# Performance work log

Hardware: AMD Instinct MI355X
Metric: run time of the kernel (lower is better)

## Reference

```python
import jax, jax.numpy as jnp
import numpy as np

D_MODEL = 2048
N_HEADS = 16
D_K = D_MODEL // N_HEADS
D_FF = 5504
SEQ = 4096
CONTEXT_LENGTH = 4096
THETA = 10000.0
EPS = 1e-5


def _linear(x, w):
    # w: (out, in), matches torch einsum '...i,oi->...o'
    return jnp.einsum('...i,oi->...o', x, w)


def _rmsnorm(x, g):
    xf = x.astype(jnp.float32)
    rms = jnp.sqrt(jnp.mean(xf * xf, axis=-1, keepdims=True) + EPS)
    return (xf / rms * g).astype(x.dtype)


def _rope_tables():
    powers = jnp.arange(0, D_K, 2, dtype=jnp.float32) / D_K
    freqs = 1.0 / (THETA ** powers)                       # (D_K/2,)
    t = jnp.arange(CONTEXT_LENGTH, dtype=jnp.float32)
    ang = jnp.outer(t, freqs)                             # (ctx, D_K/2)
    return jnp.cos(ang), jnp.sin(ang)


def _apply_rope(x, token_positions, cos_c, sin_c):
    # x: (b, h, s, d_k); token_positions: (b, s)
    cos = cos_c[token_positions][None].astype(x.dtype)    # (1, b, s, d_k/2)
    sin = sin_c[token_positions][None].astype(x.dtype)
    x_even = x[..., ::2]
    x_odd = x[..., 1::2]
    r1 = x_even * cos - x_odd * sin
    r2 = x_even * sin + x_odd * cos
    # interleave back: (..., d_k/2, 2) -> (..., d_k)
    out = jnp.stack([r1, r2], axis=-1)
    return out.reshape(x.shape)


def setup_inputs() -> dict:
    key = jax.random.key(0)
    ks = jax.random.split(key, 12)

    def w(k, out_f, in_f):
        std = (2.0 / (in_f + out_f)) ** 0.5
        return std * jax.random.normal(k, (out_f, in_f), dtype=jnp.float32)

    return {
        'x': jax.random.normal(ks[0], (1, SEQ, D_MODEL), dtype=jnp.float32),
        'w_q': w(ks[1], D_MODEL, D_MODEL),
        'w_k': w(ks[2], D_MODEL, D_MODEL),
        'w_v': w(ks[3], D_MODEL, D_MODEL),
        'w_o': w(ks[4], D_MODEL, D_MODEL),
        'w1': w(ks[5], D_FF, D_MODEL),
        'w2': w(ks[6], D_MODEL, D_FF),
        'w3': w(ks[7], D_FF, D_MODEL),
        'g1': jnp.ones((D_MODEL,), dtype=jnp.float32),
        'g2': jnp.ones((D_MODEL,), dtype=jnp.float32),
        'token_positions': jnp.broadcast_to(jnp.arange(SEQ, dtype=jnp.int32)[None, :], (1, SEQ)),
    }


def reference(x, w_q, w_k, w_v, w_o, w1, w2, w3, g1, g2, token_positions):
    b, s, _ = x.shape
    cos_c, sin_c = _rope_tables()

    # --- pre-norm attention ---
    xn = _rmsnorm(x, g1)
    def heads(t):
        return t.reshape(b, s, N_HEADS, D_K).transpose(0, 2, 1, 3)  # (b,h,s,d)
    q = heads(_linear(xn, w_q))
    k = heads(_linear(xn, w_k))
    v = heads(_linear(xn, w_v))
    q = _apply_rope(q, token_positions, cos_c, sin_c)
    k = _apply_rope(k, token_positions, cos_c, sin_c)

    score = jnp.einsum('bhqd,bhkd->bhqk', q, k) / (D_K ** 0.5)
    causal = jnp.tril(jnp.ones((s, s), dtype=bool))
    score = jnp.where(causal, score, -jnp.inf)
    probs = jax.nn.softmax(score, axis=-1)
    attn = jnp.einsum('bhqk,bhkd->bhqd', probs, v)
    attn = attn.transpose(0, 2, 1, 3).reshape(b, s, D_MODEL)
    x = x + _linear(attn, w_o)

    # --- pre-norm SwiGLU FFN ---
    xn = _rmsnorm(x, g2)
    gate = _linear(xn, w1)
    gate = gate * jax.nn.sigmoid(gate)  # SiLU
    x = x + _linear(gate * _linear(xn, w3), w2)
    return x
```

## Files before the change

kernel.cpp:

```cpp
#include <hip/hip_runtime.h>
#include <hip/hip_bf16.h>
#include <cstdint>
#include <cstddef>

constexpr int S_   = 4096;
constexpr int DM   = 2048;
constexpr int NH   = 16;
constexpr int DK   = 128;
constexpr int DFF  = 5504;
constexpr int DFFP = 5632;
constexpr int QLD  = 3 * DM;

typedef float  f32x4 __attribute__((ext_vector_type(4)));
typedef short  s16x8 __attribute__((ext_vector_type(8)));
typedef __bf16 bfx8  __attribute__((ext_vector_type(8)));

template <typename T, typename U>
__device__ inline auto mfma_try(T a, T b, f32x4 c, int)
    -> decltype(__builtin_amdgcn_mfma_f32_16x16x32_bf16(a, b, c, 0, 0, 0)) {
  return __builtin_amdgcn_mfma_f32_16x16x32_bf16(a, b, c, 0, 0, 0);
}
template <typename T, typename U>
__device__ inline f32x4 mfma_try(T a, T b, f32x4 c, long) {
  U a2 = __builtin_bit_cast(U, a);
  U b2 = __builtin_bit_cast(U, b);
  return __builtin_amdgcn_mfma_f32_16x16x32_bf16(a2, b2, c, 0, 0, 0);
}
__device__ __forceinline__ f32x4 MFMA_BF16(s16x8 a, s16x8 b, f32x4 c) {
  return mfma_try<s16x8, bfx8>(a, b, c, 0);
}

__device__ __forceinline__ void async_ld16(void* lds, const void* g) {
  __builtin_amdgcn_global_load_lds(
      (__attribute__((address_space(1))) void*)(g),
      (__attribute__((address_space(3))) void*)(lds), 16, 0, 0);
}

__device__ __forceinline__ float bf2f(__hip_bfloat16 h) { return __bfloat162float(h); }
__device__ __forceinline__ __hip_bfloat16 f2bf(float f) { return __float2bfloat16(f); }

__global__ __launch_bounds__(256) void cvt_kernel(const float* __restrict__ in,
                                                  __hip_bfloat16* __restrict__ out, int n) {
  int i = (blockIdx.x * 256 + threadIdx.x) * 4;
  if (i >= n) return;
  float4 v = *reinterpret_cast<const float4*>(in + i);
  union { __hip_bfloat16 h[4]; uint2 u; } pk;
  pk.h[0] = f2bf(v.x); pk.h[1] = f2bf(v.y); pk.h[2] = f2bf(v.z); pk.h[3] = f2bf(v.w);
  *reinterpret_cast<uint2*>(out + i) = pk.u;
}

__global__ __launch_bounds__(256) void cvt_pad_kernel(const float* __restrict__ in,
                                                      __hip_bfloat16* __restrict__ out,
                                                      int n_src, int n_tot) {
  int i = (blockIdx.x * 256 + threadIdx.x) * 4;
  if (i >= n_tot) return;
  union { __hip_bfloat16 h[4]; uint2 u; } pk;
  if (i < n_src) {
    float4 v = *reinterpret_cast<const float4*>(in + i);
    pk.h[0] = f2bf(v.x); pk.h[1] = f2bf(v.y); pk.h[2] = f2bf(v.z); pk.h[3] = f2bf(v.w);
  } else {
    pk.u.x = 0u; pk.u.y = 0u;
  }
  *reinterpret_cast<uint2*>(out + i) = pk.u;
}

__global__ __launch_bounds__(256) void rmsnorm_kernel(const float* __restrict__ x,
                                                      const float* __restrict__ g,
                                                      __hip_bfloat16* __restrict__ out) {
  const int row = blockIdx.x, tid = threadIdx.x;
  const float4* xr = reinterpret_cast<const float4*>(x + (size_t)row * DM);
  float4 a = xr[tid], b = xr[tid + 256];
  float ss = a.x*a.x + a.y*a.y + a.z*a.z + a.w*a.w
           + b.x*b.x + b.y*b.y + b.z*b.z + b.w*b.w;
#pragma unroll
  for (int off = 1; off < 64; off <<= 1) ss += __shfl_xor(ss, off);
  __shared__ float red[4];
  if ((tid & 63) == 0) red[tid >> 6] = ss;
  __syncthreads();
  const float inv = rsqrtf((red[0] + red[1] + red[2] + red[3]) * (1.0f / DM) + 1e-5f);
  const float4* gr = reinterpret_cast<const float4*>(g);
  float4 ga = gr[tid], gb = gr[tid + 256];
  union { __hip_bfloat16 h[4]; uint2 u; } pa, pb;
  pa.h[0] = f2bf(a.x * inv * ga.x); pa.h[1] = f2bf(a.y * inv * ga.y);
  pa.h[2] = f2bf(a.z * inv * ga.z); pa.h[3] = f2bf(a.w * inv * ga.w);
  pb.h[0] = f2bf(b.x * inv * gb.x); pb.h[1] = f2bf(b.y * inv * gb.y);
  pb.h[2] = f2bf(b.z * inv * gb.z); pb.h[3] = f2bf(b.w * inv * gb.w);
  uint2* o = reinterpret_cast<uint2*>(out + (size_t)row * DM);
  o[tid] = pa.u; o[tid + 256] = pb.u;
}

__global__ __launch_bounds__(256) void rope_kernel(__hip_bfloat16* __restrict__ t,
                                                   const int* __restrict__ pos, int col0) {
  const size_t idx = (size_t)blockIdx.x * 256 + threadIdx.x;
  const int j = (int)(idx & 63);
  const int h = (int)((idx >> 6) & 15);
  const int s = (int)(idx >> 10);
  const float p = (float)pos[s];
  const float freq = exp2f((float)j * (-13.287712379549449f / 64.0f));
  float sn, cs;
  sincosf(p * freq, &sn, &cs);
  __hip_bfloat16* ptr = t + (size_t)s * QLD + col0 + h * DK + 2 * j;
  const float e = bf2f(ptr[0]), o = bf2f(ptr[1]);
  ptr[0] = f2bf(e * cs - o * sn);
  ptr[1] = f2bf(e * sn + o * cs);
}

__global__ __launch_bounds__(256) void transpose_v(const __hip_bfloat16* __restrict__ qkv,
                                                   __hip_bfloat16* __restrict__ vt) {
  __shared__ __hip_bfloat16 tile[64][65];
  const int h = blockIdx.z;
  const int s0 = blockIdx.x * 64, d0 = blockIdx.y * 64;
  const int lane = threadIdx.x & 63, w = threadIdx.x >> 6;
#pragma unroll
  for (int i = 0; i < 16; i++) {
    const int r = w * 16 + i;
    tile[r][lane] = qkv[(size_t)(s0 + r) * QLD + 2 * DM + h * DK + d0 + lane];
  }
  __syncthreads();
#pragma unroll
  for (int i = 0; i < 16; i++) {
    const int r = w * 16 + i;
    vt[(size_t)(h * DK + d0 + r) * S_ + s0 + lane] = tile[lane][r];
  }
}

enum { EP_BF16 = 0, EP_SILU = 1, EP_MUL = 2, EP_ADDF32 = 3 };

template <int EP>
__global__ __launch_bounds__(512, 2) void gemm2(const __hip_bfloat16* __restrict__ A,
                                                const __hip_bfloat16* __restrict__ B,
                                                int N, int K, int lda, int ldb,
                                                void* outp, const void* extra) {
  __shared__ char lds[3][24576];
  const int tid = threadIdx.x;
  const int wave = tid >> 6, lane = tid & 63;
  const int l15 = lane & 15, l4 = lane >> 4;
  const int wm = wave >> 2, wn = wave & 3;

  const int nbn = gridDim.x;
  const int nwg = gridDim.x * gridDim.y;
  int lin = blockIdx.y * gridDim.x + blockIdx.x;
  if ((nwg & 7) == 0) lin = (lin & 7) * (nwg >> 3) + (lin >> 3);
  const int bm = (lin / nbn) * 128;
  const int bn = (lin % nbn) * 256;

  const int NT = K >> 5;

  const int srcCh = ((tid & 3) ^ ((tid >> 3) & 3)) * 16;
  const char* Asrc  = (const char*)A + (size_t)(bm + (tid >> 2)) * lda * 2 + srcCh;
  const char* Bsrc0 = (const char*)B + (size_t)(bn + (tid >> 2)) * ldb * 2 + srcCh;
  const char* Bsrc1 = (const char*)B + (size_t)(bn + 128 + (tid >> 2)) * ldb * 2 + srcCh;
  char* const ldsA  = &lds[0][0] + wave * 1024;
  char* const ldsB0 = &lds[0][0] + 8192 + wave * 1024;
  char* const ldsB1 = &lds[0][0] + 16384 + wave * 1024;

  auto stage_a  = [&](int t, int s) { async_ld16(ldsA  + s * 24576, Asrc  + (size_t)t * 64); };
  auto stage_b0 = [&](int t, int s) { async_ld16(ldsB0 + s * 24576, Bsrc0 + (size_t)t * 64); };
  auto stage_b1 = [&](int t, int s) { async_ld16(ldsB1 + s * 24576, Bsrc1 + (size_t)t * 64); };

  const int rdch = (l4 ^ ((l15 >> 1) & 3)) * 16;
  auto rd_a = [&](int s, int mq, int f) -> s16x8 {
    return *(const s16x8*)(&lds[s][0] + (wm * 64 + mq * 32 + f * 16 + l15) * 64 + rdch);
  };
  auto rd_b = [&](int s, int nf) -> s16x8 {
    return *(const s16x8*)(&lds[s][8192] + (wn * 64 + nf * 16 + l15) * 64 + rdch);
  };

  f32x4 acc[4][4] = {};

  stage_a(0, 0); stage_b0(0, 0); stage_b1(0, 0);
  stage_a(1, 1); stage_b0(1, 1); stage_b1(1, 1);

  for (int t = 0; t < NT; t++) {
    const int s = t % 3;
    if (t + 1 < NT) { asm volatile("s_waitcnt vmcnt(3)" ::: "memory"); }
    else            { asm volatile("s_waitcnt vmcnt(0)" ::: "memory"); }
    __builtin_amdgcn_s_barrier();
    asm volatile("" ::: "memory");
    s16x8 b0 = rd_b(s, 0), b1 = rd_b(s, 1), b2 = rd_b(s, 2), b3 = rd_b(s, 3);
    s16x8 a0 = rd_a(s, 0, 0), a1 = rd_a(s, 0, 1);
    if (t + 2 < NT) { const int s2 = (t + 2) % 3; stage_a(t + 2, s2); stage_b0(t + 2, s2); }
    __builtin_amdgcn_s_barrier();
    asm volatile("" ::: "memory");
    __builtin_amdgcn_s_setprio(1);
    acc[0][0] = MFMA_BF16(a0, b0, acc[0][0]);
    acc[0][1] = MFMA_BF16(a0, b1, acc[0][1]);
    acc[0][2] = MFMA_BF16(a0, b2, acc[0][2]);
    acc[0][3] = MFMA_BF16(a0, b3, acc[0][3]);
    acc[1][0] = MFMA_BF16(a1, b0, acc[1][0]);
    acc[1][1] = MFMA_BF16(a1, b1, acc[1][1]);
    acc[1][2] = MFMA_BF16(a1, b2, acc[1][2]);
    acc[1][3] = MFMA_BF16(a1, b3, acc[1][3]);
    __builtin_amdgcn_s_setprio(0);
    s16x8 a2 = rd_a(s, 1, 0), a3 = rd_a(s, 1, 1);
    if (t + 2 < NT) stage_b1(t + 2, (t + 2) % 3);
    __builtin_amdgcn_s_barrier();
    asm volatile("" ::: "memory");
    __builtin_amdgcn_s_setprio(1);
    acc[2][0] = MFMA_BF16(a2, b0, acc[2][0]);
    acc[2][1] = MFMA_BF16(a2, b1, acc[2][1]);
    acc[2][2] = MFMA_BF16(a2, b2, acc[2][2]);
    acc[2][3] = MFMA_BF16(a2, b3, acc[2][3]);
    acc[3][0] = MFMA_BF16(a3, b0, acc[3][0]);
    acc[3][1] = MFMA_BF16(a3, b1, acc[3][1]);
    acc[3][2] = MFMA_BF16(a3, b2, acc[3][2]);
    acc[3][3] = MFMA_BF16(a3, b3, acc[3][3]);
    __builtin_amdgcn_s_setprio(0);
  }

#pragma unroll
  for (int mf = 0; mf < 4; mf++)
#pragma unroll
    for (int nf = 0; nf < 4; nf++)
#pragma unroll
      for (int r = 0; r < 4; r++) {
        const int row = bm + wm * 64 + mf * 16 + l4 * 4 + r;
        const int col = bn + wn * 64 + nf * 16 + l15;
        const size_t idx = (size_t)row * N + col;
        const float v = acc[mf][nf][r];
        if constexpr (EP == EP_BF16) {
          ((__hip_bfloat16*)outp)[idx] = f2bf(v);
        } else if constexpr (EP == EP_SILU) {
          ((__hip_bfloat16*)outp)[idx] = f2bf(v / (1.0f + __expf(-v)));
        } else if constexpr (EP == EP_MUL) {
          const float o = bf2f(((const __hip_bfloat16*)extra)[idx]);
          ((__hip_bfloat16*)outp)[idx] = f2bf(v * o);
        } else {
          ((float*)outp)[idx] = v + ((const float*)extra)[idx];
        }
      }
}

__global__ __launch_bounds__(512, 4) void attn_kernel(const __hip_bfloat16* __restrict__ qkv,
                                                      const __hip_bfloat16* __restrict__ vt,
                                                      __hip_bfloat16* __restrict__ out) {
  __shared__ char sKb[2][64 * 256];
  __shared__ char sVb[2][128 * 128];
  __shared__ char sPb[8][16 * 64];

  const int h = blockIdx.y;
  const int qtile = gridDim.x - 1 - blockIdx.x;
  const int q0 = qtile * 128;
  const int tid = threadIdx.x, wave = tid >> 6, lane = tid & 63;
  const int l15 = lane & 15, l4 = lane >> 4;
  const int qr0 = q0 + wave * 16;
  const int ntiles = qtile * 2 + 2;

  s16x8 qf[4];
  {
    const char* src = (const char*)qkv + (((size_t)(qr0 + l15)) * QLD + h * DK + l4 * 8) * 2;
#pragma unroll
    for (int ks = 0; ks < 4; ks++) qf[ks] = *(const s16x8*)(src + ks * 64);
  }

  const char* qkvK = (const char*)qkv + ((size_t)DM + h * DK) * 2;
  const char* vtH  = (const char*)vt;

  auto stage = [&](int t, int buf) {
    const int kv0 = t * 64;
#pragma unroll
    for (int a = 0; a < 2; a++) {
      const int rl = wave * 8 + a * 4 + l4;
      const int ck = l15 ^ ((a * 4 + l4) & 7);
      async_ld16(sKb[buf] + (wave * 8 + a * 4) * 256,
                 qkvK + (size_t)(kv0 + rl) * (QLD * 2) + ck * 16);
    }
#pragma unroll
    for (int a = 0; a < 2; a++) {
      const int rl = wave * 16 + a * 8 + (lane >> 3);
      const int cv = (lane & 7) ^ (lane >> 3);
      async_ld16(sVb[buf] + (wave * 16 + a * 8) * 128,
                 vtH + ((size_t)(h * DK + rl) * S_ + kv0) * 2 + cv * 16);
    }
  };

  f32x4 acc[8] = {};
  float m_ = -__builtin_inff(), l_ = 0.f;
  const float scale = 0.08838834764831845f;

  stage(0, 0);
  asm volatile("s_waitcnt vmcnt(0)" ::: "memory");
  __syncthreads();

  unsigned* sPw32 = (unsigned*)sPb[wave];
  const char* sPw = (const char*)sPb[wave];

  for (int t = 0; t < ntiles; t++) {
    const int cur = t & 1;
    if (t + 1 < ntiles) stage(t + 1, cur ^ 1);
    const char* Kt = sKb[cur];
    const char* Vt = sVb[cur];
    const int kv0 = t * 64;

#pragma unroll
    for (int hf = 0; hf < 2; hf++) {
      f32x4 st[2] = {};
#pragma unroll
      for (int sub = 0; sub < 2; sub++)
#pragma unroll
        for (int ks = 0; ks < 4; ks++) {
          s16x8 kf = *(const s16x8*)(Kt + (hf * 32 + sub * 16 + l15) * 256 +
                                     (((ks * 4 + l4) ^ (l15 & 7)) & 15) * 16);
          st[sub] = MFMA_BF16(kf, qf[ks], st[sub]);
        }
      const int qrow = qr0 + l15;
      const int kvb = kv0 + hf * 32;
      float p[8];
      float mx = -__builtin_inff();
#pragma unroll
      for (int sub = 0; sub < 2; sub++)
#pragma unroll
        for (int r = 0; r < 4; r++) {
          const int kv = kvb + sub * 16 + l4 * 4 + r;
          const float v = st[sub][r] * scale;
          const float pv = (kv <= qrow) ? v : -__builtin_inff();
          p[sub * 4 + r] = pv;
          mx = fmaxf(mx, pv);
        }
      mx = fmaxf(mx, __shfl_xor(mx, 16));
      mx = fmaxf(mx, __shfl_xor(mx, 32));
      const float nm = fmaxf(m_, mx);
      const float alpha = __expf(m_ - nm);
      m_ = nm;
      float psum = 0.f;
#pragma unroll
      for (int i = 0; i < 8; i++) {
        p[i] = __expf(p[i] - nm);
        psum += p[i];
      }
      psum += __shfl_xor(psum, 16);
      psum += __shfl_xor(psum, 32);
      l_ = l_ * alpha + psum;

#pragma unroll
      for (int sub = 0; sub < 2; sub++)
#pragma unroll
        for (int rp = 0; rp < 2; rp++) {
          union { __hip_bfloat16 hh[2]; unsigned u; } pk;
          pk.hh[0] = f2bf(p[sub * 4 + rp * 2]);
          pk.hh[1] = f2bf(p[sub * 4 + rp * 2 + 1]);
          sPw32[l15 * 16 + sub * 8 + l4 * 2 + rp] = pk.u;
        }
#pragma unroll
      for (int nt = 0; nt < 8; nt++)
#pragma unroll
        for (int r = 0; r < 4; r++) acc[nt][r] *= alpha;

      s16x8 pa = *(const s16x8*)(sPw + l15 * 64 + l4 * 16);
#pragma unroll
      for (int nt = 0; nt < 8; nt++) {
        s16x8 vb = *(const s16x8*)(Vt + (nt * 16 + l15) * 128 +
                                   (((hf * 4 + l4) ^ (l15 & 7)) & 7) * 16);
        acc[nt] = MFMA_BF16(vb, pa, acc[nt]);
      }
    }
    asm volatile("s_waitcnt vmcnt(0)" ::: "memory");
    __syncthreads();
  }

  const float rl = 1.0f / l_;
#pragma unroll
  for (int nt = 0; nt < 8; nt++) {
    union { __hip_bfloat16 hh[4]; uint2 u; } pk;
#pragma unroll
    for (int r = 0; r < 4; r++) pk.hh[r] = f2bf(acc[nt][r] * rl);
    *reinterpret_cast<uint2*>(out + (size_t)(qr0 + l15) * DM + h * DK + nt * 16 + l4 * 4) = pk.u;
  }
}

extern "C" void kernel_launch(void* const* d_in, const int* in_sizes, int n_in,
                              void* d_out, int out_size, void* d_ws, size_t ws_size,
                              hipStream_t stream) {
  const float* x   = (const float*)d_in[0];
  const float* w_q = (const float*)d_in[1];
  const float* w_k = (const float*)d_in[2];
  const float* w_v = (const float*)d_in[3];
  const float* w_o = (const float*)d_in[4];
  const float* w1  = (const float*)d_in[5];
  const float* w2  = (const float*)d_in[6];
  const float* w3  = (const float*)d_in[7];
  const float* g1  = (const float*)d_in[8];
  const float* g2  = (const float*)d_in[9];
  const int*   tp  = (const int*)d_in[10];
  float* outf = (float*)d_out;

  constexpr size_t SZ_WQKV  = (size_t)3 * DM * DM * 2;
  constexpr size_t OFF_ATTN = (size_t)DM * DM * 2;
  constexpr size_t OFF_XN   = SZ_WQKV;
  constexpr size_t OFF_A2   = OFF_XN + (size_t)S_ * DM * 2;
  constexpr size_t OFF_VT   = OFF_A2 + (size_t)S_ * QLD * 2;
  constexpr size_t WS_NEED  = OFF_VT + (size_t)NH * DK * S_ * 2;
  if (ws_size < WS_NEED) return;

  char* base = (char*)d_ws;
  __hip_bfloat16* warena = (__hip_bfloat16*)base;
  __hip_bfloat16* attnb  = (__hip_bfloat16*)(base + OFF_ATTN);
  __hip_bfloat16* xn     = (__hip_bfloat16*)(base + OFF_XN);
  __hip_bfloat16* qkv    = (__hip_bfloat16*)(base + OFF_A2);
  __hip_bfloat16* ff1    = (__hip_bfloat16*)(base + OFF_A2);
  __hip_bfloat16* vt     = (__hip_bfloat16*)(base + OFF_VT);

  const int nwq = DM * DM;
  const int nff_src = DFF * DM;
  const int nff_pad = DFFP * DM;

  cvt_kernel<<<nwq / 1024, 256, 0, stream>>>(w_q, warena, nwq);
  cvt_kernel<<<nwq / 1024, 256, 0, stream>>>(w_k, warena + (size_t)DM * DM, nwq);
  cvt_kernel<<<nwq / 1024, 256, 0, stream>>>(w_v, warena + (size_t)2 * DM * DM, nwq);
  rmsnorm_kernel<<<S_, 256, 0, stream>>>(x, g1, xn);
  gemm2<EP_BF16><<<dim3(QLD / 256, S_ / 128), 512, 0, stream>>>(xn, warena, QLD, DM, DM, DM, qkv, nullptr);
  {
    const int nrope = S_ * NH * 64;
    rope_kernel<<<nrope / 256, 256, 0, stream>>>(qkv, tp, 0);
    rope_kernel<<<nrope / 256, 256, 0, stream>>>(qkv, tp, DM);
  }
  transpose_v<<<dim3(S_ / 64, DK / 64, NH), 256, 0, stream>>>(qkv, vt);
  attn_kernel<<<dim3(S_ / 128, NH), 512, 0, stream>>>(qkv, vt, attnb);
  cvt_kernel<<<nwq / 1024, 256, 0, stream>>>(w_o, warena, nwq);
  gemm2<EP_ADDF32><<<dim3(DM / 256, S_ / 128), 512, 0, stream>>>(attnb, warena, DM, DM, DM, DM, outf, x);

  rmsnorm_kernel<<<S_, 256, 0, stream>>>(outf, g2, xn);
  cvt_pad_kernel<<<nff_pad / 1024, 256, 0, stream>>>(w1, warena, nff_src, nff_pad);
  gemm2<EP_SILU><<<dim3(DFFP / 256, S_ / 128), 512, 0, stream>>>(xn, warena, DFFP, DM, DM, DM, ff1, nullptr);
  cvt_pad_kernel<<<nff_pad / 1024, 256, 0, stream>>>(w3, warena, nff_src, nff_pad);
  gemm2<EP_MUL><<<dim3(DFFP / 256, S_ / 128), 512, 0, stream>>>(xn, warena, DFFP, DM, DM, DM, ff1, ff1);
  cvt_kernel<<<(DM * DFF) / 1024, 256, 0, stream>>>(w2, warena, DM * DFF);
  gemm2<EP_ADDF32><<<dim3(DM / 256, S_ / 128), 512, 0, stream>>>(ff1, warena, DM, DFF, DFFP, DFF, outf, outf);
}
```

Before: 832.4 us.

## Rewrite attention kernel with 32x32 MFMA, register-shuffled P, lazy rescale

The flash-attention kernel moves from 16x16x32 to 32x32x16 bf16 MFMA, with 4 waves of 256 threads each owning 32 query rows instead of 8 waves owning 16. P is passed from the score layout to the PV operand through cross-half-wave shuffles rather than an LDS round trip. The accumulator rescale is skipped when the running max grows by at most 8, and MFMA sections get raised scheduling priority. V moves to a single buffer loaded after PV with extra barriers, which may expose load latency and adds register pressure from the larger accumulators.

```diff
diff --git a/kernel.cpp b/kernel.cpp
--- a/kernel.cpp
+++ b/kernel.cpp
@@ -11,9 +11,10 @@
 constexpr int DFFP = 5632;
 constexpr int QLD  = 3 * DM;
 
-typedef float  f32x4 __attribute__((ext_vector_type(4)));
-typedef short  s16x8 __attribute__((ext_vector_type(8)));
-typedef __bf16 bfx8  __attribute__((ext_vector_type(8)));
+typedef float  f32x4  __attribute__((ext_vector_type(4)));
+typedef float  f32x16 __attribute__((ext_vector_type(16)));
+typedef short  s16x8  __attribute__((ext_vector_type(8)));
+typedef __bf16 bfx8   __attribute__((ext_vector_type(8)));
 
 template <typename T, typename U>
 __device__ inline auto mfma_try(T a, T b, f32x4 c, int)
@@ -28,6 +29,21 @@
 }
 __device__ __forceinline__ f32x4 MFMA_BF16(s16x8 a, s16x8 b, f32x4 c) {
   return mfma_try<s16x8, bfx8>(a, b, c, 0);
+}
+
+template <typename T, typename U>
+__device__ inline auto mfma32_try(T a, T b, f32x16 c, int)
+    -> decltype(__builtin_amdgcn_mfma_f32_32x32x16_bf16(a, b, c, 0, 0, 0)) {
+  return __builtin_amdgcn_mfma_f32_32x32x16_bf16(a, b, c, 0, 0, 0);
+}
+template <typename T, typename U>
+__device__ inline f32x16 mfma32_try(T a, T b, f32x16 c, long) {
+  U a2 = __builtin_bit_cast(U, a);
+  U b2 = __builtin_bit_cast(U, b);
+  return __builtin_amdgcn_mfma_f32_32x32x16_bf16(a2, b2, c, 0, 0, 0);
+}
+__device__ __forceinline__ f32x16 MFMA32(s16x8 a, s16x8 b, f32x16 c) {
+  return mfma32_try<s16x8, bfx8>(a, b, c, 0);
 }
 
 __device__ __forceinline__ void async_ld16(void* lds, const void* g) {
@@ -231,141 +247,175 @@
       }
 }
 
-__global__ __launch_bounds__(512, 4) void attn_kernel(const __hip_bfloat16* __restrict__ qkv,
+__global__ __launch_bounds__(256, 2) void attn_kernel(const __hip_bfloat16* __restrict__ qkv,
                                                       const __hip_bfloat16* __restrict__ vt,
                                                       __hip_bfloat16* __restrict__ out) {
-  __shared__ char sKb[2][64 * 256];
-  __shared__ char sVb[2][128 * 128];
-  __shared__ char sPb[8][16 * 64];
+  __shared__ char sK[2][64 * 256];
+  __shared__ char sV[128 * 128];
 
   const int h = blockIdx.y;
   const int qtile = gridDim.x - 1 - blockIdx.x;
   const int q0 = qtile * 128;
   const int tid = threadIdx.x, wave = tid >> 6, lane = tid & 63;
-  const int l15 = lane & 15, l4 = lane >> 4;
-  const int qr0 = q0 + wave * 16;
+  const int l31 = lane & 31, hi = lane >> 5;
+  const int qr = q0 + wave * 32 + l31;
   const int ntiles = qtile * 2 + 2;
 
-  s16x8 qf[4];
+  s16x8 qf[8];
   {
-    const char* src = (const char*)qkv + (((size_t)(qr0 + l15)) * QLD + h * DK + l4 * 8) * 2;
-#pragma unroll
-    for (int ks = 0; ks < 4; ks++) qf[ks] = *(const s16x8*)(src + ks * 64);
+    const char* qsrc = (const char*)qkv + (size_t)qr * (QLD * 2) + h * DK * 2 + hi * 16;
+#pragma unroll
+    for (int s = 0; s < 8; s++) qf[s] = *(const s16x8*)(qsrc + s * 32);
   }
 
   const char* qkvK = (const char*)qkv + ((size_t)DM + h * DK) * 2;
-  const char* vtH  = (const char*)vt;
-
-  auto stage = [&](int t, int buf) {
+  const char* vtH  = (const char*)vt + (size_t)h * DK * S_ * 2;
+
+  auto stage_K = [&](int t, int buf) {
     const int kv0 = t * 64;
 #pragma unroll
-    for (int a = 0; a < 2; a++) {
-      const int rl = wave * 8 + a * 4 + l4;
-      const int ck = l15 ^ ((a * 4 + l4) & 7);
-      async_ld16(sKb[buf] + (wave * 8 + a * 4) * 256,
+    for (int a = 0; a < 4; a++) {
+      const int rl = wave * 16 + a * 4 + (lane >> 4);
+      const int ck = (lane & 15) ^ (rl & 7);
+      async_ld16(sK[buf] + (wave * 16 + a * 4) * 256,
                  qkvK + (size_t)(kv0 + rl) * (QLD * 2) + ck * 16);
     }
-#pragma unroll
-    for (int a = 0; a < 2; a++) {
-      const int rl = wave * 16 + a * 8 + (lane >> 3);
-      const int cv = (lane & 7) ^ (lane >> 3);
-      async_ld16(sVb[buf] + (wave * 16 + a * 8) * 128,
-                 vtH + ((size_t)(h * DK + rl) * S_ + kv0) * 2 + cv * 16);
-    }
   };
-
-  f32x4 acc[8] = {};
+  auto stage_V = [&](int t) {
+    const int kv0 = t * 64;
+#pragma unroll
+    for (int a = 0; a < 4; a++) {
+      const int rl = wave * 32 + a * 8 + (lane >> 3);
+      const int cv = (lane & 7) ^ (rl & 7);
+      async_ld16(sV + (wave * 32 + a * 8) * 128,
+                 vtH + ((size_t)rl * S_ + kv0) * 2 + cv * 16);
+    }
+  };
+
+  f32x16 acc[4] = {};
   float m_ = -__builtin_inff(), l_ = 0.f;
   const float scale = 0.08838834764831845f;
 
-  stage(0, 0);
-  asm volatile("s_waitcnt vmcnt(0)" ::: "memory");
-  __syncthreads();
-
-  unsigned* sPw32 = (unsigned*)sPb[wave];
-  const char* sPw = (const char*)sPb[wave];
-
+  stage_K(0, 0);
+  stage_V(0);
+  asm volatile("s_waitcnt vmcnt(4)" ::: "memory");
+  __builtin_amdgcn_s_barrier();
+
+  int kbuf = 0;
   for (int t = 0; t < ntiles; t++) {
-    const int cur = t & 1;
-    if (t + 1 < ntiles) stage(t + 1, cur ^ 1);
-    const char* Kt = sKb[cur];
-    const char* Vt = sVb[cur];
-    const int kv0 = t * 64;
-
-#pragma unroll
-    for (int hf = 0; hf < 2; hf++) {
-      f32x4 st[2] = {};
-#pragma unroll
-      for (int sub = 0; sub < 2; sub++)
-#pragma unroll
-        for (int ks = 0; ks < 4; ks++) {
-          s16x8 kf = *(const s16x8*)(Kt + (hf * 32 + sub * 16 + l15) * 256 +
-                                     (((ks * 4 + l4) ^ (l15 & 7)) & 15) * 16);
-          st[sub] = MFMA_BF16(kf, qf[ks], st[sub]);
-        }
-      const int qrow = qr0 + l15;
-      const int kvb = kv0 + hf * 32;
-      float p[8];
-      float mx = -__builtin_inff();
-#pragma unroll
-      for (int sub = 0; sub < 2; sub++)
-#pragma unroll
-        for (int r = 0; r < 4; r++) {
-          const int kv = kvb + sub * 16 + l4 * 4 + r;
-          const float v = st[sub][r] * scale;
-          const float pv = (kv <= qrow) ? v : -__builtin_inff();
-          p[sub * 4 + r] = pv;
-          mx = fmaxf(mx, pv);
-        }
-      mx = fmaxf(mx, __shfl_xor(mx, 16));
-      mx = fmaxf(mx, __shfl_xor(mx, 32));
+    if (t + 1 < ntiles) stage_K(t + 1, kbuf ^ 1);
+    const char* Kt = sK[kbuf];
+
+    f32x16 st0 = {}, st1 = {};
+    __builtin_amdgcn_s_setprio(1);
+#pragma unroll
+    for (int s = 0; s < 8; s++) {
+      const int cc = s * 2 + hi;
+      const int cs = (cc & 8) | ((cc ^ l31) & 7);
+      s16x8 k0 = *(const s16x8*)(Kt + l31 * 256 + cs * 16);
+      s16x8 k1 = *(const s16x8*)(Kt + (32 + l31) * 256 + cs * 16);
+      st0 = MFMA32(k0, qf[s], st0);
+      st1 = MFMA32(k1, qf[s], st1);
+    }
+    __builtin_amdgcn_s_setprio(0);
+
+    const int kvb = t * 64;
+    float p[32];
+    float mx = -__builtin_inff();
+#pragma unroll
+    for (int r = 0; r < 16; r++) {
+      const int kv = kvb + (r & 3) + 8 * (r >> 2) + 4 * hi;
+      const float v0 = st0[r] * scale;
+      const float v1 = st1[r] * scale;
+      p[r]      = (kv <= qr)      ? v0 : -__builtin_inff();
+      p[16 + r] = (kv + 32 <= qr) ? v1 : -__builtin_inff();
+      mx = fmaxf(mx, fmaxf(p[r], p[16 + r]));
+    }
+    mx = fmaxf(mx, __shfl_xor(mx, 32));
+    const bool skip = __all(mx - m_ <= 8.0f);
+    float alpha = 1.0f;
+    if (!skip) {
       const float nm = fmaxf(m_, mx);
-      const float alpha = __expf(m_ - nm);
+      alpha = __expf(m_ - nm);
       m_ = nm;
-      float psum = 0.f;
-#pragma unroll
-      for (int i = 0; i < 8; i++) {
-        p[i] = __expf(p[i] - nm);
-        psum += p[i];
-      }
-      psum += __shfl_xor(psum, 16);
-      psum += __shfl_xor(psum, 32);
-      l_ = l_ * alpha + psum;
-
-#pragma unroll
-      for (int sub = 0; sub < 2; sub++)
+#pragma unroll
+      for (int dt = 0; dt < 4; dt++)
+#pragma unroll
+        for (int r = 0; r < 16; r++) acc[dt][r] *= alpha;
+    }
+    float psum = 0.f;
+#pragma unroll
+    for (int i = 0; i < 32; i++) {
+      p[i] = __expf(p[i] - m_);
+      psum += p[i];
+    }
+    psum += __shfl_xor(psum, 32);
+    l_ = l_ * alpha + psum;
+
+    unsigned ps[16];
+#pragma unroll
+    for (int h2 = 0; h2 < 2; h2++)
+#pragma unroll
+      for (int t2 = 0; t2 < 4; t2++)
 #pragma unroll
         for (int rp = 0; rp < 2; rp++) {
           union { __hip_bfloat16 hh[2]; unsigned u; } pk;
-          pk.hh[0] = f2bf(p[sub * 4 + rp * 2]);
-          pk.hh[1] = f2bf(p[sub * 4 + rp * 2 + 1]);
-          sPw32[l15 * 16 + sub * 8 + l4 * 2 + rp] = pk.u;
+          pk.hh[0] = f2bf(p[h2 * 16 + t2 * 4 + rp * 2]);
+          pk.hh[1] = f2bf(p[h2 * 16 + t2 * 4 + rp * 2 + 1]);
+          ps[h2 * 8 + t2 * 2 + rp] = pk.u;
         }
-#pragma unroll
-      for (int nt = 0; nt < 8; nt++)
-#pragma unroll
-        for (int r = 0; r < 4; r++) acc[nt][r] *= alpha;
-
-      s16x8 pa = *(const s16x8*)(sPw + l15 * 64 + l4 * 16);
-#pragma unroll
-      for (int nt = 0; nt < 8; nt++) {
-        s16x8 vb = *(const s16x8*)(Vt + (nt * 16 + l15) * 128 +
-                                   (((hf * 4 + l4) ^ (l15 & 7)) & 7) * 16);
-        acc[nt] = MFMA_BF16(vb, pa, acc[nt]);
+
+    if (t + 1 < ntiles) { asm volatile("s_waitcnt vmcnt(4)" ::: "memory"); }
+    else                { asm volatile("s_waitcnt vmcnt(0)" ::: "memory"); }
+    __builtin_amdgcn_s_barrier();
+
+#pragma unroll
+    for (int s = 0; s < 4; s++) {
+      const int h2 = s >> 1;
+      const int iA = h2 * 8 + (2 * (s & 1)) * 2;
+      const int iB = h2 * 8 + (2 * (s & 1) + 1) * 2;
+      const unsigned keep0 = hi ? ps[iB]     : ps[iA];
+      const unsigned keep1 = hi ? ps[iB + 1] : ps[iA + 1];
+      const unsigned send0 = hi ? ps[iA]     : ps[iB];
+      const unsigned send1 = hi ? ps[iA + 1] : ps[iB + 1];
+      const unsigned recv0 = __shfl_xor(send0, 32);
+      const unsigned recv1 = __shfl_xor(send1, 32);
+      union { unsigned u[4]; s16x8 v; } fr;
+      fr.u[0] = hi ? recv0 : keep0;
+      fr.u[1] = hi ? recv1 : keep1;
+      fr.u[2] = hi ? keep0 : recv0;
+      fr.u[3] = hi ? keep1 : recv1;
+      const s16x8 pa = fr.v;
+      __builtin_amdgcn_s_setprio(1);
+#pragma unroll
+      for (int dt = 0; dt < 4; dt++) {
+        s16x8 vf = *(const s16x8*)(sV + (dt * 32 + l31) * 128 +
+                                   (((s * 2 + hi) ^ (l31 & 7)) & 7) * 16);
+        acc[dt] = MFMA32(vf, pa, acc[dt]);
       }
-    }
-    asm volatile("s_waitcnt vmcnt(0)" ::: "memory");
-    __syncthreads();
+      __builtin_amdgcn_s_setprio(0);
+    }
+
+    __builtin_amdgcn_s_barrier();
+    if (t + 1 < ntiles) {
+      stage_V(t + 1);
+      asm volatile("s_waitcnt vmcnt(4)" ::: "memory");
+      __builtin_amdgcn_s_barrier();
+    }
+    kbuf ^= 1;
   }
 
   const float rl = 1.0f / l_;
-#pragma unroll
-  for (int nt = 0; nt < 8; nt++) {
-    union { __hip_bfloat16 hh[4]; uint2 u; } pk;
-#pragma unroll
-    for (int r = 0; r < 4; r++) pk.hh[r] = f2bf(acc[nt][r] * rl);
-    *reinterpret_cast<uint2*>(out + (size_t)(qr0 + l15) * DM + h * DK + nt * 16 + l4 * 4) = pk.u;
-  }
+  __hip_bfloat16* orow = out + (size_t)qr * DM + h * DK;
+#pragma unroll
+  for (int dt = 0; dt < 4; dt++)
+#pragma unroll
+    for (int rq = 0; rq < 4; rq++) {
+      union { __hip_bfloat16 hh[4]; uint2 u; } pk;
+#pragma unroll
+      for (int e = 0; e < 4; e++) pk.hh[e] = f2bf(acc[dt][rq * 4 + e] * rl);
+      *reinterpret_cast<uint2*>(orow + dt * 32 + 8 * rq + 4 * hi) = pk.u;
+    }
 }
 
 extern "C" void kernel_launch(void* const* d_in, const int* in_sizes, int n_in,
@@ -415,7 +465,7 @@
     rope_kernel<<<nrope / 256, 256, 0, stream>>>(qkv, tp, DM);
   }
   transpose_v<<<dim3(S_ / 64, DK / 64, NH), 256, 0, stream>>>(qkv, vt);
-  attn_kernel<<<dim3(S_ / 128, NH), 512, 0, stream>>>(qkv, vt, attnb);
+  attn_kernel<<<dim3(S_ / 128, NH), 256, 0, stream>>>(qkv, vt, attnb);
   cvt_kernel<<<nwq / 1024, 256, 0, stream>>>(w_o, warena, nwq);
   gemm2<EP_ADDF32><<<dim3(DM / 256, S_ / 128), 512, 0, stream>>>(attnb, warena, DM, DM, DM, DM, outf, x);
 
```

After: 798.4 us. 1.04x faster.
